# Optimization experiments

Hardware: AMD Instinct MI355X
Metric: run time of the kernel (lower is better)

## Reference

```python
import jax, jax.numpy as jnp
import numpy as np

N, E, H = 100000, 640000, 64
DIN_N, DIN_E, L, OUT = 32, 16, 2, 1
BN_EPS = 1e-5


def setup_inputs() -> dict:
    key = jax.random.key(0)
    ks = iter(jax.random.split(key, 40))
    def p(shape, s=0.05):
        return jax.random.normal(next(ks), shape, dtype=jnp.float32) * s
    return {
        "x": jax.random.normal(next(ks), (N, DIN_N), dtype=jnp.float32),
        "edge_attr": jax.random.normal(next(ks), (E, DIN_E), dtype=jnp.float32),
        "src": jax.random.randint(next(ks), (E,), 0, N),
        "dst": jax.random.randint(next(ks), (E,), 0, N),
        "node_emb_w": p((DIN_N, H)), "node_emb_b": p((H,)),
        "edge_emb_w": p((DIN_E, H)), "edge_emb_b": p((H,)),
        "lin_edge_w": p((L, H, H)), "lin_edge_b": p((L, H)),
        "conv_w1": p((L, H, H)), "conv_b1": p((L, H)),
        "conv_w2": p((L, H, H)), "conv_b2": p((L, H)),
        "emlp_w1": p((L, 3 * H, H)), "emlp_b1": p((L, H)),
        "emlp_w2": p((L, H, H)), "emlp_b2": p((L, H)),
        "bn_gamma": jnp.ones((L, H), jnp.float32),
        "bn_beta": jnp.zeros((L, H), jnp.float32),
        "mlp_w1": p((3 * H, 50)), "mlp_b1": p((50,)),
        "mlp_w2": p((50, 25)), "mlp_b2": p((25,)),
        "mlp_w3": p((25, OUT)), "mlp_b3": p((OUT,)),
    }


def _batchnorm(h, gamma, beta):
    # training-mode BatchNorm1d over the node axis (biased variance)
    mu = jnp.mean(h, axis=0)
    var = jnp.mean(jnp.square(h - mu), axis=0)
    return gamma * (h - mu) * jax.lax.rsqrt(var + BN_EPS) + beta


def _forward(x, edge_attr, src, dst,
             node_emb_w, node_emb_b, edge_emb_w, edge_emb_b,
             lin_edge_w, lin_edge_b, conv_w1, conv_b1, conv_w2, conv_b2,
             emlp_w1, emlp_b1, emlp_w2, emlp_b2, bn_gamma, bn_beta,
             mlp_w1, mlp_b1, mlp_w2, mlp_b2, mlp_w3, mlp_b3):
    x = x @ node_emb_w + node_emb_b                       # [N, H]
    e = edge_attr @ edge_emb_w + edge_emb_b               # [E, H]
    for i in range(L):
        # GINEConv (eps=0): msg = ReLU(x_src + Lin(edge_attr)); sum at dst
        msg = jax.nn.relu(x[src] + e @ lin_edge_w[i] + lin_edge_b[i])
        agg = jax.ops.segment_sum(msg, dst, num_segments=N)
        h = x + agg
        h = jax.nn.relu(h @ conv_w1[i] + conv_b1[i]) @ conv_w2[i] + conv_b2[i]
        x = (x + jax.nn.relu(_batchnorm(h, bn_gamma[i], bn_beta[i]))) / 2
        cat = jnp.concatenate([x[src], x[dst], e], axis=-1)  # [E, 3H]
        upd = jax.nn.relu(cat @ emlp_w1[i] + emlp_b1[i]) @ emlp_w2[i] + emlp_b2[i]
        e = e + upd / 2
    # edge readout: relu(cat(x_src, x_dst)) ++ edge_attr -> MLP (dropout off/eval)
    er = jnp.concatenate(
        [jax.nn.relu(jnp.concatenate([x[src], x[dst]], axis=-1)), e], axis=-1)
    hmid = jax.nn.relu(er @ mlp_w1 + mlp_b1)
    hmid = jax.nn.relu(hmid @ mlp_w2 + mlp_b2)
    logit = hmid @ mlp_w3 + mlp_b3
    return x, logit


def reference(x, edge_attr, src, dst,
              node_emb_w, node_emb_b, edge_emb_w, edge_emb_b,
              lin_edge_w, lin_edge_b, conv_w1, conv_b1, conv_w2, conv_b2,
              emlp_w1, emlp_b1, emlp_w2, emlp_b2, bn_gamma, bn_beta,
              mlp_w1, mlp_b1, mlp_w2, mlp_b2, mlp_w3, mlp_b3):
    return _forward(x, edge_attr, src, dst,
                    node_emb_w, node_emb_b, edge_emb_w, edge_emb_b,
                    lin_edge_w, lin_edge_b, conv_w1, conv_b1, conv_w2, conv_b2,
                    emlp_w1, emlp_b1, emlp_w2, emlp_b2, bn_gamma, bn_beta,
                    mlp_w1, mlp_b1, mlp_w2, mlp_b2, mlp_w3, mlp_b3)
```

## Files before the change

### kernel.cpp

```cpp
#include <hip/hip_runtime.h>

#define NN 100000
#define NE 640000

typedef __attribute__((ext_vector_type(8))) short short8;
typedef __attribute__((ext_vector_type(4))) float f32x4;
typedef __attribute__((ext_vector_type(4))) ushort ushort4v;

__device__ __forceinline__ float bf2f(ushort u) {
    unsigned v = ((unsigned)u) << 16;
    return __builtin_bit_cast(float, v);
}
__device__ __forceinline__ ushort f2bf(float f) {
    unsigned u = __builtin_bit_cast(unsigned, f);
    u += 0x7fffu + ((u >> 16) & 1u);
    return (ushort)(u >> 16);
}
__device__ __forceinline__ short8 brelu(short8 v) {
    #pragma unroll
    for (int i = 0; i < 8; ++i) v[i] = (v[i] < (short)0) ? (short)0 : v[i];
    return v;
}

__global__ void k_w_subtile(const float* __restrict__ w, ushort* __restrict__ out,
                            int K, int Nin)
{
    int t = blockIdx.x * 256 + threadIdx.x;
    if (t >= K * 64) return;
    int k = t >> 6, c = t & 63;
    float v = (c < Nin) ? w[k * Nin + c] : 0.f;
    out[((k >> 3) * 64 + c) * 8 + (k & 7)] = f2bf(v);
}

__global__ void k_w_padk(const float* __restrict__ w, ushort* __restrict__ out,
                         int Kreal, int Kpad)
{
    int t = blockIdx.x * 256 + threadIdx.x;
    if (t >= Kpad * 64) return;
    int k = t >> 6, c = t & 63;
    float v = (k < Kreal) ? w[k * 64 + c] : 0.f;
    out[((k >> 3) * 64 + c) * 8 + (k & 7)] = f2bf(v);
}

__global__ void k_w_msg(const float* __restrict__ lw, ushort* __restrict__ out)
{
    int t = blockIdx.x * 256 + threadIdx.x;
    if (t >= 128 * 64) return;
    int k = t >> 6, c = t & 63;
    float v = (k < 64) ? (k == c ? 1.f : 0.f) : lw[(k - 64) * 64 + c];
    out[((k >> 3) * 64 + c) * 8 + (k & 7)] = f2bf(v);
}

__global__ __launch_bounds__(256) void k_node_emb_mfma(
    const float* __restrict__ xin, const ushort* __restrict__ ws,
    const float* __restrict__ b, float* __restrict__ xout,
    ushort* __restrict__ xb)
{
    __shared__ ushort wl[32 * 64];
    __shared__ float fbuf[4][16 * 64];
    __shared__ ushort bbuf[4][16 * 64];
    int tid = threadIdx.x;
    *(short8*)&wl[tid * 8] = *(const short8*)&ws[tid * 8];
    __syncthreads();

    int wid = tid >> 6, lane = tid & 63, c = lane & 15, kg = lane >> 4;
    int t = blockIdx.x * 4 + wid;
    if (t >= NN / 16) return;
    int n0 = t * 16;

    const float* xr = xin + (size_t)(n0 + c) * 32 + kg * 8;
    f32x4 u0 = *(const f32x4*)xr, u1 = *(const f32x4*)(xr + 4);
    short8 a;
    #pragma unroll
    for (int j = 0; j < 4; ++j) { a[j] = (short)f2bf(u0[j]); a[4 + j] = (short)f2bf(u1[j]); }

    f32x4 acc[4];
    #pragma unroll
    for (int nt = 0; nt < 4; ++nt) {
        float bv = b[nt * 16 + c];
        acc[nt] = f32x4{bv, bv, bv, bv};
        short8 bf = *(const short8*)&wl[(kg * 64 + nt * 16 + c) * 8];
        acc[nt] = __builtin_amdgcn_mfma_f32_16x16x32_bf16(a, bf, acc[nt], 0, 0, 0);
    }
    #pragma unroll
    for (int nt = 0; nt < 4; ++nt)
        #pragma unroll
        for (int i = 0; i < 4; ++i) {
            int rr = kg * 4 + i, cc = nt * 16 + c;
            float v = acc[nt][i];
            fbuf[wid][rr * 64 + cc] = v;
            bbuf[wid][rr * 64 + cc] = f2bf(v);
        }
    #pragma unroll
    for (int r = 0; r < 4; ++r) {
        int q = r * 64 + lane;
        *(f32x4*)&xout[(size_t)(n0 + (q >> 4)) * 64 + (q & 15) * 4] =
            *(f32x4*)&fbuf[wid][q * 4];
    }
    #pragma unroll
    for (int r = 0; r < 2; ++r) {
        int q = r * 64 + lane;
        *(short8*)&xb[(size_t)(n0 + (q >> 3)) * 64 + (q & 7) * 8] =
            *(short8*)&bbuf[wid][q * 8];
    }
}

__global__ __launch_bounds__(256) void k_edge_emb_mfma(
    const float* __restrict__ ein, const ushort* __restrict__ ws,
    const float* __restrict__ b, ushort* __restrict__ eb)
{
    __shared__ ushort wl[32 * 64];
    __shared__ ushort bbuf[4][16 * 64];
    int tid = threadIdx.x;
    *(short8*)&wl[tid * 8] = *(const short8*)&ws[tid * 8];
    __syncthreads();

    int wid = tid >> 6, lane = tid & 63, c = lane & 15, kg = lane >> 4;
    int t = blockIdx.x * 4 + wid;
    int e0 = t * 16;

    short8 a = (short8)0;
    if (kg < 2) {
        const float* er = ein + (size_t)(e0 + c) * 16 + kg * 8;
        f32x4 u0 = *(const f32x4*)er, u1 = *(const f32x4*)(er + 4);
        #pragma unroll
        for (int j = 0; j < 4; ++j) { a[j] = (short)f2bf(u0[j]); a[4 + j] = (short)f2bf(u1[j]); }
    }
    f32x4 acc[4];
    #pragma unroll
    for (int nt = 0; nt < 4; ++nt) {
        float bv = b[nt * 16 + c];
        acc[nt] = f32x4{bv, bv, bv, bv};
        short8 bf = *(const short8*)&wl[(kg * 64 + nt * 16 + c) * 8];
        acc[nt] = __builtin_amdgcn_mfma_f32_16x16x32_bf16(a, bf, acc[nt], 0, 0, 0);
    }
    #pragma unroll
    for (int nt = 0; nt < 4; ++nt)
        #pragma unroll
        for (int i = 0; i < 4; ++i)
            bbuf[wid][(kg * 4 + i) * 64 + nt * 16 + c] = f2bf(acc[nt][i]);
    #pragma unroll
    for (int r = 0; r < 2; ++r) {
        int q = r * 64 + lane;
        *(short8*)&eb[(size_t)(e0 + (q >> 3)) * 64 + (q & 7) * 8] =
            *(short8*)&bbuf[wid][q * 8];
    }
}

__global__ __launch_bounds__(256) void k_msg_mfma(
    const ushort* __restrict__ xb, const ushort* __restrict__ eb,
    const int* __restrict__ src, const int* __restrict__ dst,
    const ushort* __restrict__ wms, const float* __restrict__ lb,
    float* __restrict__ agg)
{
    __shared__ ushort wl[128 * 64];
    int tid = threadIdx.x;
    #pragma unroll
    for (int i = 0; i < 4; ++i)
        *(short8*)&wl[(i * 256 + tid) * 8] = *(const short8*)&wms[(i * 256 + tid) * 8];
    __syncthreads();

    int wid = tid >> 6, lane = tid & 63;
    int c = lane & 15, kg = lane >> 4;
    float bv[4];
    #pragma unroll
    for (int nt = 0; nt < 4; ++nt) bv[nt] = lb[nt * 16 + c];

    #pragma unroll 1
    for (int t4 = 0; t4 < 4; ++t4) {
        int e0 = blockIdx.x * 256 + wid * 64 + t4 * 16;
        int myedge = e0 + c;
        const ushort* xs = xb + (size_t)src[myedge] * 64;
        const ushort* ee = eb + (size_t)myedge * 64;
        short8 a[4];
        a[0] = *(const short8*)(xs + kg * 8);
        a[1] = *(const short8*)(xs + 32 + kg * 8);
        a[2] = *(const short8*)(ee + kg * 8);
        a[3] = *(const short8*)(ee + 32 + kg * 8);

        f32x4 acc[4];
        #pragma unroll
        for (int nt = 0; nt < 4; ++nt) acc[nt] = f32x4{bv[nt], bv[nt], bv[nt], bv[nt]};
        #pragma unroll
        for (int ks = 0; ks < 4; ++ks) {
            #pragma unroll
            for (int nt = 0; nt < 4; ++nt) {
                short8 bf = *(const short8*)&wl[((ks * 4 + kg) * 64 + nt * 16 + c) * 8];
                acc[nt] = __builtin_amdgcn_mfma_f32_16x16x32_bf16(a[ks], bf, acc[nt], 0, 0, 0);
            }
        }
        int drow[4];
        #pragma unroll
        for (int i = 0; i < 4; ++i) drow[i] = dst[e0 + kg * 4 + i];
        #pragma unroll
        for (int nt = 0; nt < 4; ++nt) {
            #pragma unroll
            for (int i = 0; i < 4; ++i) {
                float m = fmaxf(acc[nt][i], 0.f);
                unsafeAtomicAdd(&agg[(size_t)drow[i] * 64 + nt * 16 + c], m);
            }
        }
    }
}

__global__ __launch_bounds__(256) void k_conv_mfma(
    const float* __restrict__ x, float* __restrict__ hio,
    const ushort* __restrict__ w1s, const float* __restrict__ b1,
    const ushort* __restrict__ w2s, const float* __restrict__ b2,
    float* __restrict__ stats)
{
    __shared__ ushort w1l[64 * 64];
    __shared__ ushort w2l[64 * 64];
    __shared__ ushort h1l[4][1024];
    __shared__ float red[2][4][64];
    int tid = threadIdx.x;
    #pragma unroll
    for (int i = 0; i < 2; ++i) {
        *(short8*)&w1l[(i * 256 + tid) * 8] = *(const short8*)&w1s[(i * 256 + tid) * 8];
        *(short8*)&w2l[(i * 256 + tid) * 8] = *(const short8*)&w2s[(i * 256 + tid) * 8];
    }
    __syncthreads();

    int wid = tid >> 6, lane = tid & 63;
    int c = lane & 15, kg = lane >> 4;

    short8 w2f[2][4];
    #pragma unroll
    for (int ks = 0; ks < 2; ++ks)
        #pragma unroll
        for (int nt = 0; nt < 4; ++nt)
            w2f[ks][nt] = *(const short8*)&w2l[((ks * 4 + kg) * 64 + nt * 16 + c) * 8];

    float b1v[4], b2v[4];
    #pragma unroll
    for (int nt = 0; nt < 4; ++nt) { b1v[nt] = b1[nt * 16 + c]; b2v[nt] = b2[nt * 16 + c]; }

    float s1[4] = {0.f, 0.f, 0.f, 0.f}, s2[4] = {0.f, 0.f, 0.f, 0.f};
    ushort* hl = h1l[wid];

    int t = blockIdx.x * 4 + wid;
    if (t < NN / 16) {
        int n0 = t * 16;
        const float* xr = x + (size_t)(n0 + c) * 64;
        const float* hr = hio + (size_t)(n0 + c) * 64;
        short8 a[2];
        #pragma unroll
        for (int ks = 0; ks < 2; ++ks) {
            f32x4 u0 = *(const f32x4*)(xr + ks * 32 + kg * 8);
            f32x4 u1 = *(const f32x4*)(xr + ks * 32 + kg * 8 + 4);
            f32x4 v0 = *(const f32x4*)(hr + ks * 32 + kg * 8);
            f32x4 v1 = *(const f32x4*)(hr + ks * 32 + kg * 8 + 4);
            #pragma unroll
            for (int j = 0; j < 4; ++j) {
                a[ks][j]     = (short)f2bf(u0[j] + v0[j]);
                a[ks][4 + j] = (short)f2bf(u1[j] + v1[j]);
            }
        }
        f32x4 acc[4];
        #pragma unroll
        for (int nt = 0; nt < 4; ++nt) acc[nt] = f32x4{b1v[nt], b1v[nt], b1v[nt], b1v[nt]};
        #pragma unroll
        for (int ks = 0; ks < 2; ++ks) {
            #pragma unroll
            for (int nt = 0; nt < 4; ++nt) {
                short8 bf = *(const short8*)&w1l[((ks * 4 + kg) * 64 + nt * 16 + c) * 8];
                acc[nt] = __builtin_amdgcn_mfma_f32_16x16x32_bf16(a[ks], bf, acc[nt], 0, 0, 0);
            }
        }
        #pragma unroll
        for (int nt = 0; nt < 4; ++nt) {
            #pragma unroll
            for (int i = 0; i < 4; ++i) {
                int rr = kg * 4 + i, cc = nt * 16 + c;
                hl[((cc >> 3) * 16 + rr) * 8 + (cc & 7)] = f2bf(fmaxf(acc[nt][i], 0.f));
            }
        }
        f32x4 acc2[4];
        #pragma unroll
        for (int nt = 0; nt < 4; ++nt) acc2[nt] = f32x4{b2v[nt], b2v[nt], b2v[nt], b2v[nt]};
        #pragma unroll
        for (int ks = 0; ks < 2; ++ks) {
            short8 ha = *(const short8*)&hl[((ks * 4 + kg) * 16 + c) * 8];
            #pragma unroll
            for (int nt = 0; nt < 4; ++nt)
                acc2[nt] = __builtin_amdgcn_mfma_f32_16x16x32_bf16(ha, w2f[ks][nt], acc2[nt], 0, 0, 0);
        }
        #pragma unroll
        for (int nt = 0; nt < 4; ++nt) {
            #pragma unroll
            for (int i = 0; i < 4; ++i) {
                int rr = kg * 4 + i, cc = nt * 16 + c;
                float h2 = acc2[nt][i];
                hio[(size_t)(n0 + rr) * 64 + cc] = h2;
                s1[nt] += h2;
                s2[nt] += h2 * h2;
            }
        }
    }
    #pragma unroll
    for (int nt = 0; nt < 4; ++nt) {
        float v1 = s1[nt], v2 = s2[nt];
        v1 += __shfl_xor(v1, 16); v1 += __shfl_xor(v1, 32);
        v2 += __shfl_xor(v2, 16); v2 += __shfl_xor(v2, 32);
        s1[nt] = v1; s2[nt] = v2;
    }
    if (lane < 16) {
        #pragma unroll
        for (int nt = 0; nt < 4; ++nt) {
            red[0][wid][nt * 16 + c] = s1[nt];
            red[1][wid][nt * 16 + c] = s2[nt];
        }
    }
    __syncthreads();
    if (wid == 0) {
        float a = red[0][0][lane] + red[0][1][lane] + red[0][2][lane] + red[0][3][lane];
        float b = red[1][0][lane] + red[1][1][lane] + red[1][2][lane] + red[1][3][lane];
        unsafeAtomicAdd(&stats[lane], a);
        unsafeAtomicAdd(&stats[64 + lane], b);
    }
}

__global__ void k_bnfin(float* __restrict__ stats,
                        const float* __restrict__ gamma,
                        const float* __restrict__ beta)
{
    int j = threadIdx.x;
    float mu = stats[j] * (1.f / NN);
    float var = stats[64 + j] * (1.f / NN) - mu * mu;
    float a = gamma[j] * rsqrtf(var + 1e-5f);
    stats[128 + j] = a;
    stats[192 + j] = beta[j] - mu * a;
}

__global__ __launch_bounds__(256) void k_xupd4(float* __restrict__ x,
                                               const float* __restrict__ h,
                                               const float* __restrict__ stats,
                                               ushort* __restrict__ xb)
{
    int idx = blockIdx.x * 256 + threadIdx.x;
    int j4 = (idx & 15) * 4;
    f32x4 hv = *(const f32x4*)&h[(size_t)idx * 4];
    f32x4 xv = *(const f32x4*)&x[(size_t)idx * 4];
    f32x4 av = *(const f32x4*)&stats[128 + j4];
    f32x4 cv = *(const f32x4*)&stats[192 + j4];
    f32x4 xo;
    ushort4v bo;
    #pragma unroll
    for (int i = 0; i < 4; ++i) {
        float r = fmaxf(fmaf(hv[i], av[i], cv[i]), 0.f);
        float xn = (xv[i] + r) * 0.5f;
        xo[i] = xn;
        bo[i] = f2bf(xn);
    }
    *(f32x4*)&x[(size_t)idx * 4] = xo;
    *(ushort4v*)&xb[(size_t)idx * 4] = bo;
}

__global__ __launch_bounds__(256) void k_emlp_mfma(
    const ushort* __restrict__ xb, ushort* __restrict__ eb,
    const int* __restrict__ src, const int* __restrict__ dst,
    const ushort* __restrict__ w1s, const float* __restrict__ b1,
    const ushort* __restrict__ w2s, const float* __restrict__ b2)
{
    __shared__ ushort w1l[192 * 64];
    __shared__ ushort w2l[64 * 64];
    __shared__ ushort h1l[4][1024];
    int tid = threadIdx.x;
    #pragma unroll
    for (int i = 0; i < 6; ++i)
        *(short8*)&w1l[(i * 256 + tid) * 8] = *(const short8*)&w1s[(i * 256 + tid) * 8];
    #pragma unroll
    for (int i = 0; i < 2; ++i)
        *(short8*)&w2l[(i * 256 + tid) * 8] = *(const short8*)&w2s[(i * 256 + tid) * 8];
    __syncthreads();

    int wid = tid >> 6, lane = tid & 63;
    int c = lane & 15, kg = lane >> 4;

    short8 w2f[2][4];
    #pragma unroll
    for (int ks = 0; ks < 2; ++ks)
        #pragma unroll
        for (int nt = 0; nt < 4; ++nt)
            w2f[ks][nt] = *(const short8*)&w2l[((ks * 4 + kg) * 64 + nt * 16 + c) * 8];

    float b1v[4], b2v[4];
    #pragma unroll
    for (int nt = 0; nt < 4; ++nt) { b1v[nt] = b1[nt * 16 + c]; b2v[nt] = b2[nt * 16 + c]; }

    ushort* hl = h1l[wid];

    #pragma unroll 1
    for (int t4 = 0; t4 < 4; ++t4) {
        int e0 = blockIdx.x * 256 + wid * 64 + t4 * 16;
        int myedge = e0 + c;
        int s = src[myedge], d = dst[myedge];
        const ushort* xs = xb + (size_t)s * 64;
        const ushort* xd = xb + (size_t)d * 64;
        const ushort* ee = eb + (size_t)myedge * 64;
        short8 a[6];
        a[0] = *(const short8*)(xs + kg * 8);
        a[1] = *(const short8*)(xs + 32 + kg * 8);
        a[2] = *(const short8*)(xd + kg * 8);
        a[3] = *(const short8*)(xd + 32 + kg * 8);
        a[4] = *(const short8*)(ee + kg * 8);
        a[5] = *(const short8*)(ee + 32 + kg * 8);

        f32x4 acc[4];
        #pragma unroll
        for (int nt = 0; nt < 4; ++nt) acc[nt] = f32x4{b1v[nt], b1v[nt], b1v[nt], b1v[nt]};
        #pragma unroll
        for (int ks = 0; ks < 6; ++ks) {
            #pragma unroll
            for (int nt = 0; nt < 4; ++nt) {
                short8 bf = *(const short8*)&w1l[((ks * 4 + kg) * 64 + nt * 16 + c) * 8];
                acc[nt] = __builtin_amdgcn_mfma_f32_16x16x32_bf16(a[ks], bf, acc[nt], 0, 0, 0);
            }
        }
        #pragma unroll
        for (int nt = 0; nt < 4; ++nt) {
            #pragma unroll
            for (int i = 0; i < 4; ++i) {
                int rr = kg * 4 + i, cc = nt * 16 + c;
                hl[((cc >> 3) * 16 + rr) * 8 + (cc & 7)] = f2bf(fmaxf(acc[nt][i], 0.f));
            }
        }
        f32x4 acc2[4];
        #pragma unroll
        for (int nt = 0; nt < 4; ++nt) acc2[nt] = f32x4{b2v[nt], b2v[nt], b2v[nt], b2v[nt]};
        #pragma unroll
        for (int ks = 0; ks < 2; ++ks) {
            short8 ha = *(const short8*)&hl[((ks * 4 + kg) * 16 + c) * 8];
            #pragma unroll
            for (int nt = 0; nt < 4; ++nt)
                acc2[nt] = __builtin_amdgcn_mfma_f32_16x16x32_bf16(ha, w2f[ks][nt], acc2[nt], 0, 0, 0);
        }
        #pragma unroll
        for (int nt = 0; nt < 4; ++nt) {
            #pragma unroll
            for (int i = 0; i < 4; ++i) {
                int rr = kg * 4 + i, cc = nt * 16 + c;
                size_t off = (size_t)(e0 + rr) * 64 + cc;
                eb[off] = f2bf(bf2f(eb[off]) + 0.5f * acc2[nt][i]);
            }
        }
    }
}

__global__ __launch_bounds__(256) void k_readout_mfma(
    const ushort* __restrict__ xb, const ushort* __restrict__ eb,
    const int* __restrict__ src, const int* __restrict__ dst,
    const ushort* __restrict__ w1s, const float* __restrict__ b1,
    const float* __restrict__ w2, const float* __restrict__ b2,
    const float* __restrict__ w3, const float* __restrict__ b3,
    float* __restrict__ logit)
{
    __shared__ ushort w1l[192 * 64];
    __shared__ ushort hw[4][64 * 50];
    int tid = threadIdx.x;
    #pragma unroll
    for (int i = 0; i < 6; ++i)
        *(short8*)&w1l[(i * 256 + tid) * 8] = *(const short8*)&w1s[(i * 256 + tid) * 8];
    __syncthreads();

    int wid = tid >> 6, lane = tid & 63;
    int c = lane & 15, kg = lane >> 4;
    float b1v[4];
    #pragma unroll
    for (int nt = 0; nt < 4; ++nt) b1v[nt] = (nt * 16 + c < 50) ? b1[nt * 16 + c] : 0.f;

    #pragma unroll 1
    for (int t4 = 0; t4 < 4; ++t4) {
        int e0 = blockIdx.x * 256 + wid * 64 + t4 * 16;
        int myedge = e0 + c;
        int s = src[myedge], d = dst[myedge];
        const ushort* xs = xb + (size_t)s * 64;
        const ushort* xd = xb + (size_t)d * 64;
        const ushort* ee = eb + (size_t)myedge * 64;
        short8 a[6];
        a[0] = brelu(*(const short8*)(xs + kg * 8));
        a[1] = brelu(*(const short8*)(xs + 32 + kg * 8));
        a[2] = brelu(*(const short8*)(xd + kg * 8));
        a[3] = brelu(*(const short8*)(xd + 32 + kg * 8));
        a[4] = *(const short8*)(ee + kg * 8);
        a[5] = *(const short8*)(ee + 32 + kg * 8);

        f32x4 acc[4];
        #pragma unroll
        for (int nt = 0; nt < 4; ++nt) acc[nt] = f32x4{b1v[nt], b1v[nt], b1v[nt], b1v[nt]};
        #pragma unroll
        for (int ks = 0; ks < 6; ++ks) {
            #pragma unroll
            for (int nt = 0; nt < 4; ++nt) {
                short8 bf = *(const short8*)&w1l[((ks * 4 + kg) * 64 + nt * 16 + c) * 8];
                acc[nt] = __builtin_amdgcn_mfma_f32_16x16x32_bf16(a[ks], bf, acc[nt], 0, 0, 0);
            }
        }
        #pragma unroll
        for (int nt = 0; nt < 4; ++nt) {
            #pragma unroll
            for (int i = 0; i < 4; ++i) {
                int rr = kg * 4 + i, cc = nt * 16 + c;
                if (cc < 50)
                    hw[wid][(t4 * 16 + rr) * 50 + cc] = f2bf(fmaxf(acc[nt][i], 0.f));
            }
        }
    }
    int edge = blockIdx.x * 256 + wid * 64 + lane;
    const ushort* hrow = &hw[wid][lane * 50];
    float a25[25];
    #pragma unroll
    for (int j = 0; j < 25; ++j) a25[j] = b2[j];
    #pragma unroll 2
    for (int k = 0; k < 50; ++k) {
        float hv = bf2f(hrow[k]);
        #pragma unroll
        for (int j = 0; j < 25; ++j) a25[j] = fmaf(hv, w2[k * 25 + j], a25[j]);
    }
    float lg = b3[0];
    #pragma unroll
    for (int k = 0; k < 25; ++k) lg = fmaf(fmaxf(a25[k], 0.f), w3[k], lg);
    logit[edge] = lg;
}

extern "C" void kernel_launch(void* const* d_in, const int* in_sizes, int n_in,
                              void* d_out, int out_size, void* d_ws, size_t ws_size,
                              hipStream_t stream)
{
    const float* x_in  = (const float*)d_in[0];
    const float* eattr = (const float*)d_in[1];
    const int*   src   = (const int*)d_in[2];
    const int*   dst   = (const int*)d_in[3];
    const float* n_w   = (const float*)d_in[4];
    const float* n_b   = (const float*)d_in[5];
    const float* e_w   = (const float*)d_in[6];
    const float* e_b   = (const float*)d_in[7];
    const float* lw    = (const float*)d_in[8];
    const float* lb    = (const float*)d_in[9];
    const float* cw1   = (const float*)d_in[10];
    const float* cb1   = (const float*)d_in[11];
    const float* cw2   = (const float*)d_in[12];
    const float* cb2   = (const float*)d_in[13];
    const float* ew1   = (const float*)d_in[14];
    const float* eb1   = (const float*)d_in[15];
    const float* ew2   = (const float*)d_in[16];
    const float* eb2   = (const float*)d_in[17];
    const float* gam   = (const float*)d_in[18];
    const float* bet   = (const float*)d_in[19];
    const float* m1w   = (const float*)d_in[20];
    const float* m1b   = (const float*)d_in[21];
    const float* m2w   = (const float*)d_in[22];
    const float* m2b   = (const float*)d_in[23];
    const float* m3w   = (const float*)d_in[24];
    const float* m3b   = (const float*)d_in[25];

    float* xbuf  = (float*)d_out;
    float* logit = xbuf + (size_t)NN * 64;

    ushort* eb    = (ushort*)d_ws;
    float*  tmp   = (float*)(eb + (size_t)NE * 64);
    float*  stats = tmp + (size_t)NN * 64;
    ushort* w1s   = (ushort*)(stats + 256);
    ushort* w2s   = w1s + 2 * 192 * 64;
    ushort* m1s   = w2s + 2 * 64 * 64;
    ushort* xb    = m1s + 192 * 64;
    ushort* wms   = xb + (size_t)NN * 64;
    ushort* cw1s  = wms + 2 * 128 * 64;
    ushort* cw2s  = cw1s + 2 * 64 * 64;
    ushort* nws   = cw2s + 2 * 64 * 64;
    ushort* ews   = nws + 32 * 64;

    k_w_subtile<<<48, 256, 0, stream>>>(ew1,            w1s,            192, 64);
    k_w_subtile<<<48, 256, 0, stream>>>(ew1 + 192 * 64, w1s + 192 * 64, 192, 64);
    k_w_subtile<<<16, 256, 0, stream>>>(ew2,            w2s,            64, 64);
    k_w_subtile<<<16, 256, 0, stream>>>(ew2 + 64 * 64,  w2s + 64 * 64,  64, 64);
    k_w_subtile<<<48, 256, 0, stream>>>(m1w,            m1s,            192, 50);
    k_w_msg<<<32, 256, 0, stream>>>(lw,           wms);
    k_w_msg<<<32, 256, 0, stream>>>(lw + 64 * 64, wms + 128 * 64);
    k_w_subtile<<<16, 256, 0, stream>>>(cw1,            cw1s,           64, 64);
    k_w_subtile<<<16, 256, 0, stream>>>(cw1 + 64 * 64,  cw1s + 64 * 64, 64, 64);
    k_w_subtile<<<16, 256, 0, stream>>>(cw2,            cw2s,           64, 64);
    k_w_subtile<<<16, 256, 0, stream>>>(cw2 + 64 * 64,  cw2s + 64 * 64, 64, 64);
    k_w_padk<<<8, 256, 0, stream>>>(n_w, nws, 32, 32);
    k_w_padk<<<8, 256, 0, stream>>>(e_w, ews, 16, 32);

    k_node_emb_mfma<<<(NN / 16 + 3) / 4, 256, 0, stream>>>(x_in, nws, n_b, xbuf, xb);
    k_edge_emb_mfma<<<NE / 64, 256, 0, stream>>>(eattr, ews, e_b, eb);

    for (int l = 0; l < 2; ++l) {
        hipMemsetAsync(tmp, 0, (size_t)NN * 64 * sizeof(float), stream);
        hipMemsetAsync(stats, 0, 256 * sizeof(float), stream);
        k_msg_mfma<<<NE / 256, 256, 0, stream>>>(xb, eb, src, dst,
                                                 wms + l * 128 * 64, lb + l * 64, tmp);
        k_conv_mfma<<<(NN / 16 + 3) / 4, 256, 0, stream>>>(
            xbuf, tmp, cw1s + l * 64 * 64, cb1 + l * 64,
            cw2s + l * 64 * 64, cb2 + l * 64, stats);
        k_bnfin<<<1, 64, 0, stream>>>(stats, gam + l * 64, bet + l * 64);
        k_xupd4<<<NN * 16 / 256, 256, 0, stream>>>(xbuf, tmp, stats, xb);
        k_emlp_mfma<<<NE / 256, 256, 0, stream>>>(xb, eb, src, dst,
                                                  w1s + l * 192 * 64, eb1 + l * 64,
                                                  w2s + l * 64 * 64, eb2 + l * 64);
    }

    k_readout_mfma<<<NE / 256, 256, 0, stream>>>(xb, eb, src, dst,
                                                 m1s, m1b, m2w, m2b, m3w, m3b, logit);
}
```

Before: 659.0 us.

## Replace atomic scatter aggregation with dst-sorted CSR gather fused into conv

Builds a CSR grouping of edges by destination (histogram, scan, scatter) on every call. The message kernel then writes bf16 messages in sorted order, and the conv kernel reduces each node's messages before its MLP. This removes the float atomics into a zeroed aggregation buffer and the per-layer memset. In exchange it adds several preprocessing kernels, a large message buffer, and an edge-count-dependent loop with divergent per-lane lengths, and it rounds messages to bf16 before summing.

```diff
diff --git a/kernel.cpp b/kernel.cpp
--- a/kernel.cpp
+++ b/kernel.cpp
@@ -2,6 +2,7 @@
 
 #define NN 100000
 #define NE 640000
+#define NB_SCAN 98
 
 typedef __attribute__((ext_vector_type(8))) short short8;
 typedef __attribute__((ext_vector_type(4))) float f32x4;
@@ -20,6 +21,68 @@
     #pragma unroll
     for (int i = 0; i < 8; ++i) v[i] = (v[i] < (short)0) ? (short)0 : v[i];
     return v;
+}
+
+__global__ void k_hist(const int* __restrict__ dst, int* __restrict__ hist)
+{
+    int i = blockIdx.x * 256 + threadIdx.x;
+    atomicAdd(&hist[dst[i]], 1);
+}
+
+__global__ __launch_bounds__(256) void k_scan_part(const int* __restrict__ hist,
+                                                   int* __restrict__ rp,
+                                                   int* __restrict__ parts)
+{
+    __shared__ int s[256];
+    int b = blockIdx.x, t = threadIdx.x;
+    int base = b * 1024 + t * 4;
+    int v[4]; int sum = 0;
+    #pragma unroll
+    for (int i = 0; i < 4; ++i) { int idx = base + i; v[i] = (idx < NN) ? hist[idx] : 0; sum += v[i]; }
+    s[t] = sum; __syncthreads();
+    for (int off = 1; off < 256; off <<= 1) {
+        int x = (t >= off) ? s[t - off] : 0;
+        __syncthreads(); s[t] += x; __syncthreads();
+    }
+    int excl = s[t] - sum;
+    if (t == 255) parts[b] = s[255];
+    int run = excl;
+    #pragma unroll
+    for (int i = 0; i < 4; ++i) { int idx = base + i; if (idx < NN) rp[idx] = run; run += v[i]; }
+}
+
+__global__ void k_scan_tops(int* __restrict__ parts, int* __restrict__ rp)
+{
+    __shared__ int s[128];
+    int t = threadIdx.x;
+    int v = (t < NB_SCAN) ? parts[t] : 0;
+    s[t] = v; __syncthreads();
+    for (int off = 1; off < 128; off <<= 1) {
+        int x = (t >= off) ? s[t - off] : 0;
+        __syncthreads(); s[t] += x; __syncthreads();
+    }
+    parts[t] = s[t] - v;
+    if (t == 0) rp[NN] = NE;
+}
+
+__global__ __launch_bounds__(256) void k_scan_add(int* __restrict__ rp,
+                                                  const int* __restrict__ parts,
+                                                  int* __restrict__ cursor)
+{
+    int i = blockIdx.x * 256 + threadIdx.x;
+    if (i >= NN) return;
+    int v = rp[i] + parts[i >> 10];
+    rp[i] = v; cursor[i] = v;
+}
+
+__global__ void k_scatter(const int* __restrict__ src, const int* __restrict__ dst,
+                          int* __restrict__ cursor, int* __restrict__ eidx,
+                          int* __restrict__ ssrc)
+{
+    int i = blockIdx.x * 256 + threadIdx.x;
+    int d = dst[i];
+    int p = atomicAdd(&cursor[d], 1);
+    eidx[p] = i; ssrc[p] = src[i];
 }
 
 __global__ void k_w_subtile(const float* __restrict__ w, ushort* __restrict__ out,
@@ -147,13 +210,14 @@
     }
 }
 
-__global__ __launch_bounds__(256) void k_msg_mfma(
+__global__ __launch_bounds__(256) void k_msgA(
     const ushort* __restrict__ xb, const ushort* __restrict__ eb,
-    const int* __restrict__ src, const int* __restrict__ dst,
+    const int* __restrict__ eidx, const int* __restrict__ ssrc,
     const ushort* __restrict__ wms, const float* __restrict__ lb,
-    float* __restrict__ agg)
+    ushort* __restrict__ msgbuf)
 {
     __shared__ ushort wl[128 * 64];
+    __shared__ ushort bbuf[4][16 * 64];
     int tid = threadIdx.x;
     #pragma unroll
     for (int i = 0; i < 4; ++i)
@@ -168,10 +232,11 @@
 
     #pragma unroll 1
     for (int t4 = 0; t4 < 4; ++t4) {
-        int e0 = blockIdx.x * 256 + wid * 64 + t4 * 16;
-        int myedge = e0 + c;
-        const ushort* xs = xb + (size_t)src[myedge] * 64;
-        const ushort* ee = eb + (size_t)myedge * 64;
+        int p0 = blockIdx.x * 256 + wid * 64 + t4 * 16;
+        int row = p0 + c;
+        int edge = eidx[row], s = ssrc[row];
+        const ushort* xs = xb + (size_t)s * 64;
+        const ushort* ee = eb + (size_t)edge * 64;
         short8 a[4];
         a[0] = *(const short8*)(xs + kg * 8);
         a[1] = *(const short8*)(xs + 32 + kg * 8);
@@ -189,22 +254,23 @@
                 acc[nt] = __builtin_amdgcn_mfma_f32_16x16x32_bf16(a[ks], bf, acc[nt], 0, 0, 0);
             }
         }
-        int drow[4];
-        #pragma unroll
-        for (int i = 0; i < 4; ++i) drow[i] = dst[e0 + kg * 4 + i];
-        #pragma unroll
-        for (int nt = 0; nt < 4; ++nt) {
-            #pragma unroll
-            for (int i = 0; i < 4; ++i) {
-                float m = fmaxf(acc[nt][i], 0.f);
-                unsafeAtomicAdd(&agg[(size_t)drow[i] * 64 + nt * 16 + c], m);
-            }
-        }
-    }
-}
-
-__global__ __launch_bounds__(256) void k_conv_mfma(
-    const float* __restrict__ x, float* __restrict__ hio,
+        #pragma unroll
+        for (int nt = 0; nt < 4; ++nt)
+            #pragma unroll
+            for (int i = 0; i < 4; ++i)
+                bbuf[wid][(kg * 4 + i) * 64 + nt * 16 + c] = f2bf(fmaxf(acc[nt][i], 0.f));
+        #pragma unroll
+        for (int r = 0; r < 2; ++r) {
+            int q = r * 64 + lane;
+            *(short8*)&msgbuf[(size_t)(p0 + (q >> 3)) * 64 + (q & 7) * 8] =
+                *(short8*)&bbuf[wid][q * 8];
+        }
+    }
+}
+
+__global__ __launch_bounds__(256) void k_conv_csr(
+    const float* __restrict__ x, const ushort* __restrict__ msgbuf,
+    const int* __restrict__ rp, float* __restrict__ hout,
     const ushort* __restrict__ w1s, const float* __restrict__ b1,
     const ushort* __restrict__ w2s, const float* __restrict__ b2,
     float* __restrict__ stats)
@@ -241,20 +307,30 @@
     int t = blockIdx.x * 4 + wid;
     if (t < NN / 16) {
         int n0 = t * 16;
-        const float* xr = x + (size_t)(n0 + c) * 64;
-        const float* hr = hio + (size_t)(n0 + c) * 64;
+        int n = n0 + c;
+        int jb = rp[n], je = rp[n + 1];
+        float sm0[8] = {0,0,0,0,0,0,0,0}, sm1[8] = {0,0,0,0,0,0,0,0};
+        for (int j = jb; j < je; ++j) {
+            short8 m0 = *(const short8*)&msgbuf[(size_t)j * 64 + kg * 8];
+            short8 m1 = *(const short8*)&msgbuf[(size_t)j * 64 + 32 + kg * 8];
+            #pragma unroll
+            for (int i = 0; i < 8; ++i) {
+                sm0[i] += bf2f((ushort)m0[i]);
+                sm1[i] += bf2f((ushort)m1[i]);
+            }
+        }
+        const float* xr = x + (size_t)n * 64;
+        f32x4 u0 = *(const f32x4*)(xr + kg * 8);
+        f32x4 u1 = *(const f32x4*)(xr + kg * 8 + 4);
+        f32x4 v0 = *(const f32x4*)(xr + 32 + kg * 8);
+        f32x4 v1 = *(const f32x4*)(xr + 32 + kg * 8 + 4);
         short8 a[2];
         #pragma unroll
-        for (int ks = 0; ks < 2; ++ks) {
-            f32x4 u0 = *(const f32x4*)(xr + ks * 32 + kg * 8);
-            f32x4 u1 = *(const f32x4*)(xr + ks * 32 + kg * 8 + 4);
-            f32x4 v0 = *(const f32x4*)(hr + ks * 32 + kg * 8);
-            f32x4 v1 = *(const f32x4*)(hr + ks * 32 + kg * 8 + 4);
-            #pragma unroll
-            for (int j = 0; j < 4; ++j) {
-                a[ks][j]     = (short)f2bf(u0[j] + v0[j]);
-                a[ks][4 + j] = (short)f2bf(u1[j] + v1[j]);
-            }
+        for (int j = 0; j < 4; ++j) {
+            a[0][j]     = (short)f2bf(u0[j] + sm0[j]);
+            a[0][4 + j] = (short)f2bf(u1[j] + sm0[4 + j]);
+            a[1][j]     = (short)f2bf(v0[j] + sm1[j]);
+            a[1][4 + j] = (short)f2bf(v1[j] + sm1[4 + j]);
         }
         f32x4 acc[4];
         #pragma unroll
@@ -291,7 +367,7 @@
             for (int i = 0; i < 4; ++i) {
                 int rr = kg * 4 + i, cc = nt * 16 + c;
                 float h2 = acc2[nt][i];
-                hio[(size_t)(n0 + rr) * 64 + cc] = h2;
+                hout[(size_t)(n0 + rr) * 64 + cc] = h2;
                 s1[nt] += h2;
                 s2[nt] += h2 * h2;
             }
@@ -557,18 +633,32 @@
     float* xbuf  = (float*)d_out;
     float* logit = xbuf + (size_t)NN * 64;
 
-    ushort* eb    = (ushort*)d_ws;
-    float*  tmp   = (float*)(eb + (size_t)NE * 64);
-    float*  stats = tmp + (size_t)NN * 64;
-    ushort* w1s   = (ushort*)(stats + 256);
-    ushort* w2s   = w1s + 2 * 192 * 64;
-    ushort* m1s   = w2s + 2 * 64 * 64;
-    ushort* xb    = m1s + 192 * 64;
-    ushort* wms   = xb + (size_t)NN * 64;
-    ushort* cw1s  = wms + 2 * 128 * 64;
-    ushort* cw2s  = cw1s + 2 * 64 * 64;
-    ushort* nws   = cw2s + 2 * 64 * 64;
-    ushort* ews   = nws + 32 * 64;
+    ushort* eb     = (ushort*)d_ws;
+    float*  tmp    = (float*)(eb + (size_t)NE * 64);
+    float*  stats  = tmp + (size_t)NN * 64;
+    ushort* w1s    = (ushort*)(stats + 256);
+    ushort* w2s    = w1s + 2 * 192 * 64;
+    ushort* m1s    = w2s + 2 * 64 * 64;
+    ushort* xb     = m1s + 192 * 64;
+    ushort* wms    = xb + (size_t)NN * 64;
+    ushort* cw1s   = wms + 2 * 128 * 64;
+    ushort* cw2s   = cw1s + 2 * 64 * 64;
+    ushort* nws    = cw2s + 2 * 64 * 64;
+    ushort* ews    = nws + 32 * 64;
+    ushort* msgbuf = ews + 32 * 64;
+    int*    hist   = (int*)(msgbuf + (size_t)NE * 64);
+    int*    rp     = hist + NN;
+    int*    cursor = rp + NN + 1;
+    int*    parts  = cursor + NN;
+    int*    eidx   = parts + 128;
+    int*    ssrc   = eidx + NE;
+
+    hipMemsetAsync(hist, 0, NN * sizeof(int), stream);
+    k_hist<<<NE / 256, 256, 0, stream>>>(dst, hist);
+    k_scan_part<<<NB_SCAN, 256, 0, stream>>>(hist, rp, parts);
+    k_scan_tops<<<1, 128, 0, stream>>>(parts, rp);
+    k_scan_add<<<(NN + 255) / 256, 256, 0, stream>>>(rp, parts, cursor);
+    k_scatter<<<NE / 256, 256, 0, stream>>>(src, dst, cursor, eidx, ssrc);
 
     k_w_subtile<<<48, 256, 0, stream>>>(ew1,            w1s,            192, 64);
     k_w_subtile<<<48, 256, 0, stream>>>(ew1 + 192 * 64, w1s + 192 * 64, 192, 64);
@@ -588,12 +678,11 @@
     k_edge_emb_mfma<<<NE / 64, 256, 0, stream>>>(eattr, ews, e_b, eb);
 
     for (int l = 0; l < 2; ++l) {
-        hipMemsetAsync(tmp, 0, (size_t)NN * 64 * sizeof(float), stream);
         hipMemsetAsync(stats, 0, 256 * sizeof(float), stream);
-        k_msg_mfma<<<NE / 256, 256, 0, stream>>>(xb, eb, src, dst,
-                                                 wms + l * 128 * 64, lb + l * 64, tmp);
-        k_conv_mfma<<<(NN / 16 + 3) / 4, 256, 0, stream>>>(
-            xbuf, tmp, cw1s + l * 64 * 64, cb1 + l * 64,
+        k_msgA<<<NE / 256, 256, 0, stream>>>(xb, eb, eidx, ssrc,
+                                             wms + l * 128 * 64, lb + l * 64, msgbuf);
+        k_conv_csr<<<(NN / 16 + 3) / 4, 256, 0, stream>>>(
+            xbuf, msgbuf, rp, tmp, cw1s + l * 64 * 64, cb1 + l * 64,
             cw2s + l * 64 * 64, cb2 + l * 64, stats);
         k_bnfin<<<1, 64, 0, stream>>>(stats, gam + l * 64, bet + l * 64);
         k_xupd4<<<NN * 16 / 256, 256, 0, stream>>>(xbuf, tmp, stats, xb);
```

New measurement: 578.2 us. -12.3%, faster.
